# Performance work log

Measured on AMD Instinct MI355X. Metric: run time of the kernel, lower is better.

The kernel has to match this reference:

```python
import jax, jax.numpy as jnp
import numpy as np

B, D, E = 16384, 2048, 16
MIN_K, MAX_K = 1, 4
H = D // 2  # hidden width of similarity/routing MLPs
TOP20 = int(0.2 * D)  # static: int(0.2 * x.shape[-1])


def _lin_init(k, fan_in, shape):
    bound = 1.0 / np.sqrt(fan_in)
    return jax.random.uniform(k, shape, jnp.float32, -bound, bound)


def setup_inputs() -> dict:
    key = jax.random.key(0)
    ks = jax.random.split(key, 16)
    return {
        'x': jax.random.normal(ks[0], (B, D), jnp.float32),
        'expert_patterns': jax.random.normal(ks[1], (E, D), jnp.float32),
        # similarity_network: Linear(D, D//2) -> ReLU -> Linear(D//2, E)
        'Ws1': _lin_init(ks[2], D, (D, H)), 'bs1': _lin_init(ks[3], D, (H,)),
        'Ws2': _lin_init(ks[4], H, (H, E)), 'bs2': _lin_init(ks[5], H, (E,)),
        # routing_network: Linear(D+E, D//2) -> ReLU -> (Dropout eval) -> Linear(D//2, E) -> Softmax
        'Wr1': _lin_init(ks[6], D + E, (D + E, H)), 'br1': _lin_init(ks[7], D + E, (H,)),
        'Wr2': _lin_init(ks[8], H, (H, E)), 'br2': _lin_init(ks[9], H, (E,)),
        # k_predictor: Linear(6,16) -> ReLU -> Linear(16,1) -> Sigmoid
        'Wk1': _lin_init(ks[10], 6, (6, 16)), 'bk1': _lin_init(ks[11], 6, (16,)),
        'Wk2': _lin_init(ks[12], 16, (16, 1)), 'bk2': _lin_init(ks[13], 16, (1,)),
    }


def _feature_analysis(x):
    mean = jnp.mean(x, axis=-1, keepdims=True)
    var_u = jnp.var(x, axis=-1, ddof=1)  # torch.var is unbiased
    std = jnp.sqrt(var_u[:, None] + 1e-8)
    skew = jnp.mean(((x - mean) / std) ** 3, axis=-1)
    ax = jnp.abs(x)
    sorted_ax = -jnp.sort(-ax, axis=-1)  # descending
    total = jnp.sum(sorted_ax, axis=-1)
    top = jnp.sum(sorted_ax[:, :TOP20], axis=-1)
    # stacked in DynamicTopKSelector order: sparsity,variance,magnitude,norm,skewness,concentration
    stats = jnp.stack([
        jnp.mean((x == 0).astype(jnp.float32), axis=-1),
        var_u,
        jnp.max(ax, axis=-1),
        jnp.linalg.norm(x, axis=-1),
        skew,
        top / (total + 1e-8),
    ], axis=-1)  # [B, 6]
    return stats


def _lower_median(v):
    # torch.median returns the lower of two middle elements for even n
    n = v.shape[0]
    return jnp.sort(v)[(n - 1) // 2]


def reference(x, expert_patterns, Ws1, bs1, Ws2, bs2, Wr1, br1, Wr2, br2, Wk1, bk1, Wk2, bk2):
    stats = _feature_analysis(x)  # [B, 6]
    # expert specialization
    sims = x @ expert_patterns.T                                  # [B, E]
    spec = jax.nn.relu(x @ Ws1 + bs1) @ Ws2 + bs2                 # [B, E]
    spec_scores = jax.nn.sigmoid(sims + spec)
    # routing network (dropout inactive in eval)
    ri = jnp.concatenate([x, spec_scores], axis=-1)               # [B, D+E]
    probs = jax.nn.softmax(jax.nn.relu(ri @ Wr1 + br1) @ Wr2 + br2, axis=-1)
    # dynamic top-k (host-side scalar in torch -> static-shape pad/mask here)
    k_ratio = jax.nn.sigmoid(jax.nn.relu(stats @ Wk1 + bk1) @ Wk2 + bk2)[:, 0]
    k_values = MIN_K + (MAX_K - MIN_K) * k_ratio
    k = jnp.clip(jnp.floor(_lower_median(k_values)).astype(jnp.int32), MIN_K, MAX_K)
    k = jax.lax.stop_gradient(k)
    topk_probs, topk_idx = jax.lax.top_k(probs, MAX_K)            # [B, MAX_K]
    mask = jnp.arange(MAX_K) < k                                  # first k slots active
    gates = jax.nn.softmax(jnp.where(mask, topk_probs, -1e30), axis=-1)
    return gates, topk_idx, probs, stats
```

## Files before the change

### kernel.cpp

```cpp
#include <hip/hip_runtime.h>
#include <hip/hip_bf16.h>

typedef unsigned short u16;
typedef __attribute__((ext_vector_type(8))) short bf16x8;
typedef __attribute__((ext_vector_type(4))) float f32x4;

#define BB 16384
#define DD 2048
#define KEXT 2112
#define HH 1024
#define EE 16
#define TOPN 409

__device__ __forceinline__ u16 f2bf(float f) {
    union { float f; unsigned u; } c; c.f = f;
    unsigned r = c.u + 0x7fffu + ((c.u >> 16) & 1u);
    return (u16)(r >> 16);
}
__device__ __forceinline__ float bf2f(u16 h) {
    union { unsigned u; float f; } c; c.u = ((unsigned)h) << 16; return c.f;
}

__device__ __forceinline__ void ld16_lds(const void* g, void* l) {
    __builtin_amdgcn_global_load_lds(
        (const __attribute__((address_space(1))) unsigned int*)g,
        (__attribute__((address_space(3))) unsigned int*)l, 16, 0, 0);
}

__global__ __launch_bounds__(256)
void prep_t(const float* __restrict__ Ws1, const float* __restrict__ Wr1,
            u16* __restrict__ w1t, u16* __restrict__ wr1h, u16* __restrict__ wr1l,
            const float* __restrict__ Ws2, const float* __restrict__ Wr2,
            const float* __restrict__ pat,
            u16* __restrict__ w2t1, u16* __restrict__ wr2th, u16* __restrict__ wr2tl,
            u16* __restrict__ patTh, u16* __restrict__ patTl)
{
    __shared__ float tile[64][65];
    const int kt = blockIdx.x;
    const int nt = blockIdx.y;
    const int mat = blockIdx.z;
    const int t = threadIdx.x;
    if (mat == 2) {
        int idx = (kt * 16 + nt) * 256 + t;
        if (idx < EE * HH) {
            int e = idx / HH, n = idx % HH;
            w2t1[idx] = f2bf(Ws2[(size_t)n * EE + e]);
            float v = Wr2[(size_t)n * EE + e];
            u16 h = f2bf(v);
            wr2th[idx] = h;
            wr2tl[idx] = f2bf(v - bf2f(h));
        }
        if (idx < EE * DD) {
            float v = pat[idx];
            u16 h = f2bf(v);
            patTh[idx] = h;
            patTl[idx] = f2bf(v - bf2f(h));
        }
        return;
    }
    if (mat == 0 && kt >= 32) return;
    const int k0 = kt * 64, n0 = nt * 64;
    const float* src = mat ? Wr1 : Ws1;
    const int kmax = mat ? (DD + EE) : DD;
    #pragma unroll
    for (int i = 0; i < 16; ++i) {
        int e = i * 256 + t;
        int r = e >> 6, c = e & 63;
        float v = (k0 + r < kmax) ? src[(size_t)(k0 + r) * HH + n0 + c] : 0.0f;
        tile[r][c] = v;
    }
    __syncthreads();
    #pragma unroll
    for (int i = 0; i < 16; ++i) {
        int e = i * 256 + t;
        int rn = e >> 6, ck = e & 63;
        float v = tile[ck][rn];
        size_t oidx = (size_t)(n0 + rn) * KEXT + k0 + ck;
        if (mat == 0) {
            w1t[oidx] = f2bf(v);
        } else {
            u16 h = f2bf(v);
            wr1h[oidx] = h;
            wr1l[oidx] = f2bf(v - bf2f(h));
        }
    }
}

__global__ __launch_bounds__(256)
void stats_kernel(const float* __restrict__ x,
                  const float* __restrict__ Wk1, const float* __restrict__ bk1,
                  const float* __restrict__ Wk2, const float* __restrict__ bk2,
                  float* __restrict__ stats_out, u16* __restrict__ xh, u16* __restrict__ xl,
                  unsigned* __restrict__ kflags)
{
    const int wid = threadIdx.x >> 6;
    const int lane = threadIdx.x & 63;
    const int row = blockIdx.x * 4 + wid;
    const float* xr = x + (size_t)row * DD;

    float v[32];
    #pragma unroll
    for (int s = 0; s < 8; ++s) {
        float4 a = *(const float4*)(xr + s * 256 + lane * 4);
        v[s*4+0]=a.x; v[s*4+1]=a.y; v[s*4+2]=a.z; v[s*4+3]=a.w;
    }

    u16* ph = xh + (size_t)row * KEXT;
    u16* pl = xl + (size_t)row * KEXT;
    #pragma unroll
    for (int s = 0; s < 8; ++s) {
        union { u16 a[4]; unsigned long long q; } H, L;
        #pragma unroll
        for (int c = 0; c < 4; ++c) {
            float f = v[s*4+c];
            u16 h = f2bf(f);
            H.a[c] = h; L.a[c] = f2bf(f - bf2f(h));
        }
        *(unsigned long long*)(ph + s*256 + lane*4) = H.q;
        *(unsigned long long*)(pl + s*256 + lane*4) = L.q;
    }
    ph[DD + lane] = 0;
    pl[DD + lane] = 0;

    float s1 = 0;
    #pragma unroll
    for (int j = 0; j < 32; ++j) s1 += v[j];
    #pragma unroll
    for (int off = 32; off >= 1; off >>= 1) s1 += __shfl_xor(s1, off);
    const float mean = s1 * (1.0f/2048.0f);

    float s2=0, s3=0, sa=0, sq=0, zc=0, mx=0;
    #pragma unroll
    for (int j = 0; j < 32; ++j) {
        float d = v[j] - mean;
        s2 += d*d; s3 += d*d*d;
        float av = fabsf(v[j]);
        sa += av; sq += v[j]*v[j];
        mx = fmaxf(mx, av);
        zc += (v[j] == 0.0f) ? 1.0f : 0.0f;
    }
    #pragma unroll
    for (int off = 32; off >= 1; off >>= 1) {
        s2 += __shfl_xor(s2, off);
        s3 += __shfl_xor(s3, off);
        sa += __shfl_xor(sa, off);
        sq += __shfl_xor(sq, off);
        zc += __shfl_xor(zc, off);
        mx = fmaxf(mx, __shfl_xor(mx, off));
    }

    #pragma unroll
    for (int j = 0; j < 32; ++j) v[j] = fabsf(v[j]);

    unsigned lo = 0, hi = 0x7F800000u;
    while (lo < hi) {
        unsigned mid = (lo + hi) >> 1;
        float midf = __uint_as_float(mid);
        unsigned cnt = 0;
        #pragma unroll
        for (int j = 0; j < 32; ++j)
            cnt += (unsigned)__popcll(__ballot(v[j] > midf));
        if (cnt < TOPN) hi = mid; else lo = mid + 1;
    }
    const float T = __uint_as_float(lo);

    float cg = 0, sg = 0;
    #pragma unroll
    for (int j = 0; j < 32; ++j) {
        if (v[j] > T) { cg += 1.0f; sg += v[j]; }
    }
    #pragma unroll
    for (int off = 32; off >= 1; off >>= 1) { cg += __shfl_xor(cg, off); sg += __shfl_xor(sg, off); }

    if (lane == 0) {
        float top = sg + ((float)TOPN - cg) * T;
        float var_u = s2 * (1.0f/2047.0f);
        float stdv = sqrtf(var_u + 1e-8f);
        float st0 = zc * (1.0f/2048.0f);
        float st1 = var_u;
        float st2 = mx;
        float st3 = sqrtf(sq);
        float st4 = (s3 * (1.0f/2048.0f)) / (stdv*stdv*stdv);
        float st5 = top / (sa + 1e-8f);
        float* so = stats_out + (size_t)row * 6;
        so[0]=st0; so[1]=st1; so[2]=st2; so[3]=st3; so[4]=st4; so[5]=st5;
        float stv[6] = {st0,st1,st2,st3,st4,st5};
        float o = bk2[0];
        #pragma unroll
        for (int i = 0; i < 16; ++i) {
            float h = bk1[i];
            #pragma unroll
            for (int f = 0; f < 6; ++f) h += stv[f] * Wk1[f*16 + i];
            o += fmaxf(h, 0.0f) * Wk2[i];
        }
        float kr = 1.0f / (1.0f + expf(-o));
        float kv = 1.0f + 3.0f * kr;
        kflags[row] = (kv < 2.0f ? 1u : 0u) | (kv < 3.0f ? 0x10000u : 0u);
    }
}

__global__ __launch_bounds__(1024)
void kmed_kernel(const unsigned* __restrict__ kflags, int* __restrict__ counters)
{
    const int t = threadIdx.x;
    unsigned s = 0;
    for (int i = t; i < BB; i += 1024) s += kflags[i];
    #pragma unroll
    for (int off = 32; off >= 1; off >>= 1) s += __shfl_xor(s, off);
    __shared__ unsigned red[16];
    if ((t & 63) == 0) red[t >> 6] = s;
    __syncthreads();
    if (t == 0) {
        unsigned tot = 0;
        #pragma unroll
        for (int w = 0; w < 16; ++w) tot += red[w];
        counters[0] = (int)(tot & 0xFFFFu);
        counters[1] = (int)(tot >> 16);
    }
}

__global__ __launch_bounds__(256)
void gemm_h1(const u16* __restrict__ xh, const u16* __restrict__ xl,
             const u16* __restrict__ w1t, const float* __restrict__ bias,
             const u16* __restrict__ w2t,
             const u16* __restrict__ patTh, const u16* __restrict__ patTl,
             float* __restrict__ spec_part, float* __restrict__ sims_part)
{
    __shared__ u16 SM[2*8192];
    u16* AsH = SM;
    u16* BsH = SM + 8192;
    const int t = threadIdx.x;
    const int id = blockIdx.x;
    const int xcd = id & 7;
    const int jj = id >> 3;
    const int nblk = jj & 7;
    const int mgrp = jj >> 3;
    const int m0 = (xcd * 16 + mgrp) * 128;
    const int n0 = nblk * 128;
    const int wid = t >> 6, lane = t & 63, l16 = lane & 15, q = lane >> 4;
    const int wm = (wid & 1) * 64, wn = (wid >> 1) * 64;
    const int x7 = l16 & 7;
    const bool swave = (wid < 2);

    f32x4 acc[4][4] = {};
    f32x4 sacc[4] = {};

    for (int it = 0; it < 32; ++it) {
        const int k0 = it * 64;
        __syncthreads();
        #pragma unroll
        for (int s = 0; s < 4; ++s) {
            int seg = t + s * 256;
            int row = seg >> 3;
            int c = (seg & 7) ^ (row & 7);
            size_t goff = (size_t)k0 + c * 8;
            ld16_lds(xh  + (size_t)(m0 + row) * KEXT + goff, (void*)(AsH + seg * 8));
            ld16_lds(w1t + (size_t)(n0 + row) * KEXT + goff, (void*)(BsH + seg * 8));
        }
        __syncthreads();
        const bool simiter = ((it & 7) == nblk);
        #pragma unroll
        for (int h = 0; h < 2; ++h) {
            const int coff = ((4*h + q) ^ x7) * 8;
            bf16x8 afh[4], bfh[4];
            #pragma unroll
            for (int i = 0; i < 4; ++i) {
                afh[i] = *(const bf16x8*)(AsH + (wm + 16*i + l16) * 64 + coff);
                bfh[i] = *(const bf16x8*)(BsH + (wn + 16*i + l16) * 64 + coff);
            }
            #pragma unroll
            for (int i = 0; i < 4; ++i)
                #pragma unroll
                for (int j = 0; j < 4; ++j)
                    acc[i][j] = __builtin_amdgcn_mfma_f32_16x16x32_bf16(afh[i], bfh[j], acc[i][j], 0, 0, 0);
            if (simiter && swave) {
                const int gc = k0 + (4*h + q) * 8;
                bf16x8 pb0 = *(const bf16x8*)(patTh + (size_t)l16 * DD + gc);
                bf16x8 pb1 = *(const bf16x8*)(patTl + (size_t)l16 * DD + gc);
                #pragma unroll
                for (int i = 0; i < 4; ++i) {
                    bf16x8 al = *(const bf16x8*)(xl + (size_t)(m0 + wm + 16*i + l16) * KEXT + gc);
                    sacc[i] = __builtin_amdgcn_mfma_f32_16x16x32_bf16(afh[i], pb0, sacc[i], 0, 0, 0);
                    sacc[i] = __builtin_amdgcn_mfma_f32_16x16x32_bf16(afh[i], pb1, sacc[i], 0, 0, 0);
                    sacc[i] = __builtin_amdgcn_mfma_f32_16x16x32_bf16(al,     pb0, sacc[i], 0, 0, 0);
                }
            }
        }
    }

    __syncthreads();
    u16* h1t = SM;
    #pragma unroll
    for (int j = 0; j < 4; ++j) {
        int col = wn + 16*j + l16;
        float bvj = bias[n0 + col];
        #pragma unroll
        for (int i = 0; i < 4; ++i)
            #pragma unroll
            for (int r = 0; r < 4; ++r) {
                int row = wm + 16*i + q*4 + r;
                float vv = acc[i][j][r] + bvj;
                vv = vv > 0.0f ? vv : 0.0f;
                h1t[row * 128 + col] = f2bf(vv);
            }
    }
    __syncthreads();
    const int mb = wid * 32;
    f32x4 s16[2] = {};
    #pragma unroll
    for (int kk = 0; kk < 4; ++kk) {
        bf16x8 wb = *(const bf16x8*)(w2t + (size_t)l16 * HH + n0 + kk*32 + q*8);
        #pragma unroll
        for (int i2 = 0; i2 < 2; ++i2) {
            bf16x8 af = *(const bf16x8*)(h1t + (mb + i2*16 + l16) * 128 + kk*32 + q*8);
            s16[i2] = __builtin_amdgcn_mfma_f32_16x16x32_bf16(af, wb, s16[i2], 0, 0, 0);
        }
    }
    #pragma unroll
    for (int i2 = 0; i2 < 2; ++i2)
        #pragma unroll
        for (int r = 0; r < 4; ++r) {
            int row = m0 + mb + i2*16 + q*4 + r;
            spec_part[((size_t)nblk * BB + row) * EE + l16] = s16[i2][r];
        }
    if (swave) {
        #pragma unroll
        for (int i = 0; i < 4; ++i)
            #pragma unroll
            for (int r = 0; r < 4; ++r) {
                int row = m0 + wm + 16*i + q*4 + r;
                sims_part[((size_t)nblk * BB + row) * EE + l16] = sacc[i][r];
            }
    }
}

__global__ __launch_bounds__(256)
void gemm_h2(const u16* __restrict__ Ah, const u16* __restrict__ Al,
             const u16* __restrict__ Bh, const u16* __restrict__ Bl,
             const float* __restrict__ bias,
             const u16* __restrict__ wr2th, const u16* __restrict__ wr2tl,
             float* __restrict__ lg_part)
{
    __shared__ u16 SM[4*8192];
    u16* AsH = SM;
    u16* BsH = SM + 8192;
    u16* AsL = SM + 2*8192;
    u16* BsL = SM + 3*8192;
    const int t = threadIdx.x;
    const int id = blockIdx.x;
    const int xcd = id & 7;
    const int jj = id >> 3;
    const int nblk = jj & 7;
    const int mgrp = jj >> 3;
    const int m0 = (xcd * 16 + mgrp) * 128;
    const int n0 = nblk * 128;
    const int wid = t >> 6, lane = t & 63, l16 = lane & 15, q = lane >> 4;
    const int wm = (wid & 1) * 64, wn = (wid >> 1) * 64;
    const int x7 = l16 & 7;

    f32x4 acc[4][4] = {};

    for (int it = 0; it < 33; ++it) {
        const int k0 = it * 64;
        __syncthreads();
        #pragma unroll
        for (int s = 0; s < 4; ++s) {
            int seg = t + s * 256;
            int row = seg >> 3;
            int c = (seg & 7) ^ (row & 7);
            size_t goff = (size_t)k0 + c * 8;
            size_t aoff = (size_t)(m0 + row) * KEXT + goff;
            size_t boff = (size_t)(n0 + row) * KEXT + goff;
            ld16_lds(Ah + aoff, (void*)(AsH + seg * 8));
            ld16_lds(Bh + boff, (void*)(BsH + seg * 8));
            ld16_lds(Al + aoff, (void*)(AsL + seg * 8));
            ld16_lds(Bl + boff, (void*)(BsL + seg * 8));
        }
        __syncthreads();
        #pragma unroll
        for (int h = 0; h < 2; ++h) {
            const int coff = ((4*h + q) ^ x7) * 8;
            bf16x8 afh[4], bfh[4], afl[4], bfl[4];
            #pragma unroll
            for (int i = 0; i < 4; ++i) {
                const int ra = (wm + 16*i + l16) * 64 + coff;
                const int rb = (wn + 16*i + l16) * 64 + coff;
                afh[i] = *(const bf16x8*)(AsH + ra);
                bfh[i] = *(const bf16x8*)(BsH + rb);
                afl[i] = *(const bf16x8*)(AsL + ra);
                bfl[i] = *(const bf16x8*)(BsL + rb);
            }
            #pragma unroll
            for (int i = 0; i < 4; ++i)
                #pragma unroll
                for (int j = 0; j < 4; ++j) {
                    acc[i][j] = __builtin_amdgcn_mfma_f32_16x16x32_bf16(afh[i], bfh[j], acc[i][j], 0, 0, 0);
                    acc[i][j] = __builtin_amdgcn_mfma_f32_16x16x32_bf16(afh[i], bfl[j], acc[i][j], 0, 0, 0);
                    acc[i][j] = __builtin_amdgcn_mfma_f32_16x16x32_bf16(afl[i], bfh[j], acc[i][j], 0, 0, 0);
                }
        }
    }

    __syncthreads();
    u16* h2h = SM;
    u16* h2l = SM + 16384;
    #pragma unroll
    for (int j = 0; j < 4; ++j) {
        int col = wn + 16*j + l16;
        float bvj = bias[n0 + col];
        #pragma unroll
        for (int i = 0; i < 4; ++i)
            #pragma unroll
            for (int r = 0; r < 4; ++r) {
                int row = wm + 16*i + q*4 + r;
                float vv = acc[i][j][r] + bvj;
                vv = vv > 0.0f ? vv : 0.0f;
                u16 h = f2bf(vv);
                h2h[row * 128 + col] = h;
                h2l[row * 128 + col] = f2bf(vv - bf2f(h));
            }
    }
    __syncthreads();
    const int mb = wid * 32;
    f32x4 lacc[2] = {};
    #pragma unroll
    for (int kk = 0; kk < 4; ++kk) {
        bf16x8 wbh = *(const bf16x8*)(wr2th + (size_t)l16 * HH + n0 + kk*32 + q*8);
        bf16x8 wbl = *(const bf16x8*)(wr2tl + (size_t)l16 * HH + n0 + kk*32 + q*8);
        #pragma unroll
        for (int i2 = 0; i2 < 2; ++i2) {
            bf16x8 ah = *(const bf16x8*)(h2h + (mb + i2*16 + l16) * 128 + kk*32 + q*8);
            bf16x8 al = *(const bf16x8*)(h2l + (mb + i2*16 + l16) * 128 + kk*32 + q*8);
            lacc[i2] = __builtin_amdgcn_mfma_f32_16x16x32_bf16(ah, wbh, lacc[i2], 0, 0, 0);
            lacc[i2] = __builtin_amdgcn_mfma_f32_16x16x32_bf16(ah, wbl, lacc[i2], 0, 0, 0);
            lacc[i2] = __builtin_amdgcn_mfma_f32_16x16x32_bf16(al, wbh, lacc[i2], 0, 0, 0);
        }
    }
    #pragma unroll
    for (int i2 = 0; i2 < 2; ++i2)
        #pragma unroll
        for (int r = 0; r < 4; ++r) {
            int row = m0 + mb + i2*16 + q*4 + r;
            lg_part[((size_t)nblk * BB + row) * EE + l16] = lacc[i2][r];
        }
}

__global__ __launch_bounds__(64)
void thinAc(const float* __restrict__ spec_part, const float* __restrict__ sims_part,
            const float* __restrict__ bs2,
            u16* __restrict__ xh_w, u16* __restrict__ xl_w)
{
    const int lane = threadIdx.x & 63;
    const int l16 = lane & 15, q = lane >> 4;
    const int m0 = blockIdx.x * 16;
    const float b2 = bs2[l16];
    #pragma unroll
    for (int r = 0; r < 4; ++r) {
        int row = m0 + q*4 + r;
        float sp = 0.0f;
        #pragma unroll
        for (int p = 0; p < 8; ++p) {
            sp += spec_part[((size_t)p * BB + row) * EE + l16];
            sp += sims_part[((size_t)p * BB + row) * EE + l16];
        }
        float ssv = 1.0f / (1.0f + expf(-(sp + b2)));
        u16 h = f2bf(ssv);
        xh_w[(size_t)row * KEXT + DD + l16] = h;
        xl_w[(size_t)row * KEXT + DD + l16] = f2bf(ssv - bf2f(h));
    }
}

__global__ __launch_bounds__(64)
void thinBc(const float* __restrict__ lg_part,
            const float* __restrict__ br2, const int* __restrict__ counters,
            float* __restrict__ out_gates, float* __restrict__ out_idx,
            float* __restrict__ out_probs)
{
    const int lane = threadIdx.x & 63;
    const int l16 = lane & 15, q = lane >> 4;
    const int m0 = blockIdx.x * 16;
    const float b2 = br2[l16];
    const int c2 = counters[0], c3 = counters[1];
    const int k = (c2 >= 8192) ? 1 : ((c3 >= 8192) ? 2 : 3);
    #pragma unroll
    for (int r = 0; r < 4; ++r) {
        const int row = m0 + q*4 + r;
        float lg = b2;
        #pragma unroll
        for (int p = 0; p < 8; ++p)
            lg += lg_part[((size_t)p * BB + row) * EE + l16];
        float mxv = lg;
        #pragma unroll
        for (int off = 1; off < 16; off <<= 1) mxv = fmaxf(mxv, __shfl_xor(mxv, off));
        float e = expf(lg - mxv);
        float den = e;
        #pragma unroll
        for (int off = 1; off < 16; off <<= 1) den += __shfl_xor(den, off);
        float p = e / den;
        out_probs[(size_t)row * EE + l16] = p;
        int kcur = (int)((__float_as_uint(p) & ~15u) | (15u - (unsigned)l16));
        float tv[4]; int ti[4];
        #pragma unroll
        for (int s = 0; s < 4; ++s) {
            int kk = kcur;
            #pragma unroll
            for (int off = 1; off < 16; off <<= 1) kk = max(kk, __shfl_xor(kk, off));
            int widx = 15 - (kk & 15);
            ti[s] = widx;
            tv[s] = __shfl(p, q * 16 + widx);
            if (l16 == widx) kcur = 0;
        }
        float den2 = 0.0f;
        float g[4];
        #pragma unroll
        for (int s = 0; s < 4; ++s) {
            g[s] = expf(tv[s] - tv[0]);
            if (s < k) den2 += g[s];
        }
        if (l16 < 4) {
            out_gates[(size_t)row * 4 + l16] = (l16 < k) ? g[l16] / den2 : 0.0f;
            out_idx[(size_t)row * 4 + l16] = (float)ti[l16];
        }
    }
}

extern "C" void kernel_launch(void* const* d_in, const int* in_sizes, int n_in,
                              void* d_out, int out_size, void* d_ws, size_t ws_size,
                              hipStream_t stream) {
    const float* x   = (const float*)d_in[0];
    const float* pat = (const float*)d_in[1];
    const float* Ws1 = (const float*)d_in[2];
    const float* bs1 = (const float*)d_in[3];
    const float* Ws2 = (const float*)d_in[4];
    const float* bs2 = (const float*)d_in[5];
    const float* Wr1 = (const float*)d_in[6];
    const float* br1 = (const float*)d_in[7];
    const float* Wr2 = (const float*)d_in[8];
    const float* br2 = (const float*)d_in[9];
    const float* Wk1 = (const float*)d_in[10];
    const float* bk1 = (const float*)d_in[11];
    const float* Wk2 = (const float*)d_in[12];
    const float* bk2 = (const float*)d_in[13];

    char* ws = (char*)d_ws;
    size_t off = 0;
    auto alloc = [&](size_t bytes) { char* p = ws + off; off += (bytes + 255) & ~(size_t)255; return p; };
    u16* xh     = (u16*)alloc((size_t)BB * KEXT * 2);
    u16* xl     = (u16*)alloc((size_t)BB * KEXT * 2);
    u16* w1t    = (u16*)alloc((size_t)HH * KEXT * 2);
    u16* wr1h   = (u16*)alloc((size_t)HH * KEXT * 2);
    u16* wr1l   = (u16*)alloc((size_t)HH * KEXT * 2);
    u16* w2t1   = (u16*)alloc((size_t)EE * HH * 2);
    u16* wr2th  = (u16*)alloc((size_t)EE * HH * 2);
    u16* wr2tl  = (u16*)alloc((size_t)EE * HH * 2);
    u16* patTh  = (u16*)alloc((size_t)EE * DD * 2);
    u16* patTl  = (u16*)alloc((size_t)EE * DD * 2);
    float* partA = (float*)alloc((size_t)16 * BB * EE * 4);
    float* partB = (float*)alloc((size_t)8  * BB * EE * 4);
    unsigned* kflags = (unsigned*)alloc((size_t)BB * 4);
    int* cnt      = (int*)alloc(64);

    float* spec_part = partA;
    float* sims_part = partA + (size_t)8 * BB * EE;
    float* lg_part   = partB;

    float* out        = (float*)d_out;
    float* out_gates  = out;
    float* out_idx    = out + (size_t)BB * 4;
    float* out_probs  = out + (size_t)BB * 8;
    float* out_stats  = out + (size_t)BB * 24;

    prep_t<<<dim3(33, 16, 3), 256, 0, stream>>>(Ws1, Wr1, w1t, wr1h, wr1l,
        Ws2, Wr2, pat, w2t1, wr2th, wr2tl, patTh, patTl);

    stats_kernel<<<BB/4, 256, 0, stream>>>(x, Wk1, bk1, Wk2, bk2, out_stats, xh, xl, kflags);

    kmed_kernel<<<1, 1024, 0, stream>>>(kflags, cnt);

    gemm_h1<<<1024, 256, 0, stream>>>(xh, xl, w1t, bs1, w2t1, patTh, patTl,
                                      spec_part, sims_part);

    thinAc<<<BB/16, 64, 0, stream>>>(spec_part, sims_part, bs2, xh, xl);

    gemm_h2<<<1024, 256, 0, stream>>>(xh, xl, wr1h, wr1l, br1, wr2th, wr2tl, lg_part);

    thinBc<<<BB/16, 64, 0, stream>>>(lg_part, br2, cnt, out_gates, out_idx, out_probs);
}
```

Before: 570.1 us.

## Merge stats and weight prep kernels, bf16 top-k search, enlarge gemm_h1 M tile

Three unrelated changes. The weight-prep kernel and the stats kernel are merged into one launch, with the prep work placed in extra blocks after the 4096 stats blocks. The top-20% threshold binary search now runs on bf16-rounded integer keys, which cuts the iterations from about 31 to about 15. gemm_h1 goes from 128x128 to 256x128 tiles with 512 blocks and launch bounds of 2, so each B tile is reused across twice as many rows. The bf16 threshold makes the top-sum approximate when values tie near the threshold, since ties are filled at T rather than the exact value. The larger tile also raises register and LDS pressure.

```diff
diff --git a/kernel.cpp b/kernel.cpp
--- a/kernel.cpp
+++ b/kernel.cpp
@@ -28,73 +28,76 @@
 }
 
 __global__ __launch_bounds__(256)
-void prep_t(const float* __restrict__ Ws1, const float* __restrict__ Wr1,
-            u16* __restrict__ w1t, u16* __restrict__ wr1h, u16* __restrict__ wr1l,
-            const float* __restrict__ Ws2, const float* __restrict__ Wr2,
-            const float* __restrict__ pat,
-            u16* __restrict__ w2t1, u16* __restrict__ wr2th, u16* __restrict__ wr2tl,
-            u16* __restrict__ patTh, u16* __restrict__ patTl)
+void stats_prep(const float* __restrict__ x,
+                const float* __restrict__ Wk1, const float* __restrict__ bk1,
+                const float* __restrict__ Wk2, const float* __restrict__ bk2,
+                float* __restrict__ stats_out, u16* __restrict__ xh, u16* __restrict__ xl,
+                unsigned* __restrict__ kflags,
+                const float* __restrict__ Ws1, const float* __restrict__ Wr1,
+                u16* __restrict__ w1t, u16* __restrict__ wr1h, u16* __restrict__ wr1l,
+                const float* __restrict__ Ws2, const float* __restrict__ Wr2,
+                const float* __restrict__ pat,
+                u16* __restrict__ w2t1, u16* __restrict__ wr2th, u16* __restrict__ wr2tl,
+                u16* __restrict__ patTh, u16* __restrict__ patTl)
 {
     __shared__ float tile[64][65];
-    const int kt = blockIdx.x;
-    const int nt = blockIdx.y;
-    const int mat = blockIdx.z;
     const int t = threadIdx.x;
-    if (mat == 2) {
-        int idx = (kt * 16 + nt) * 256 + t;
-        if (idx < EE * HH) {
-            int e = idx / HH, n = idx % HH;
-            w2t1[idx] = f2bf(Ws2[(size_t)n * EE + e]);
-            float v = Wr2[(size_t)n * EE + e];
-            u16 h = f2bf(v);
-            wr2th[idx] = h;
-            wr2tl[idx] = f2bf(v - bf2f(h));
-        }
-        if (idx < EE * DD) {
-            float v = pat[idx];
-            u16 h = f2bf(v);
-            patTh[idx] = h;
-            patTl[idx] = f2bf(v - bf2f(h));
+
+    if (blockIdx.x >= 4096) {
+        const int e = blockIdx.x - 4096;
+        const int mat = e / (33 * 16);
+        const int rem = e % (33 * 16);
+        const int kt = rem % 33;
+        const int nt = rem / 33;
+        if (mat == 2) {
+            int idx = rem * 256 + t;
+            if (idx < EE * HH) {
+                int ee = idx / HH, n = idx % HH;
+                w2t1[idx] = f2bf(Ws2[(size_t)n * EE + ee]);
+                float v = Wr2[(size_t)n * EE + ee];
+                u16 h = f2bf(v);
+                wr2th[idx] = h;
+                wr2tl[idx] = f2bf(v - bf2f(h));
+            }
+            if (idx < EE * DD) {
+                float v = pat[idx];
+                u16 h = f2bf(v);
+                patTh[idx] = h;
+                patTl[idx] = f2bf(v - bf2f(h));
+            }
+            return;
+        }
+        if (mat == 0 && kt >= 32) return;
+        const int k0 = kt * 64, n0 = nt * 64;
+        const float* src = mat ? Wr1 : Ws1;
+        const int kmax = mat ? (DD + EE) : DD;
+        #pragma unroll
+        for (int i = 0; i < 16; ++i) {
+            int ei = i * 256 + t;
+            int r = ei >> 6, c = ei & 63;
+            float v = (k0 + r < kmax) ? src[(size_t)(k0 + r) * HH + n0 + c] : 0.0f;
+            tile[r][c] = v;
+        }
+        __syncthreads();
+        #pragma unroll
+        for (int i = 0; i < 16; ++i) {
+            int ei = i * 256 + t;
+            int rn = ei >> 6, ck = ei & 63;
+            float v = tile[ck][rn];
+            size_t oidx = (size_t)(n0 + rn) * KEXT + k0 + ck;
+            if (mat == 0) {
+                w1t[oidx] = f2bf(v);
+            } else {
+                u16 h = f2bf(v);
+                wr1h[oidx] = h;
+                wr1l[oidx] = f2bf(v - bf2f(h));
+            }
         }
         return;
     }
-    if (mat == 0 && kt >= 32) return;
-    const int k0 = kt * 64, n0 = nt * 64;
-    const float* src = mat ? Wr1 : Ws1;
-    const int kmax = mat ? (DD + EE) : DD;
-    #pragma unroll
-    for (int i = 0; i < 16; ++i) {
-        int e = i * 256 + t;
-        int r = e >> 6, c = e & 63;
-        float v = (k0 + r < kmax) ? src[(size_t)(k0 + r) * HH + n0 + c] : 0.0f;
-        tile[r][c] = v;
-    }
-    __syncthreads();
-    #pragma unroll
-    for (int i = 0; i < 16; ++i) {
-        int e = i * 256 + t;
-        int rn = e >> 6, ck = e & 63;
-        float v = tile[ck][rn];
-        size_t oidx = (size_t)(n0 + rn) * KEXT + k0 + ck;
-        if (mat == 0) {
-            w1t[oidx] = f2bf(v);
-        } else {
-            u16 h = f2bf(v);
-            wr1h[oidx] = h;
-            wr1l[oidx] = f2bf(v - bf2f(h));
-        }
-    }
-}
-
-__global__ __launch_bounds__(256)
-void stats_kernel(const float* __restrict__ x,
-                  const float* __restrict__ Wk1, const float* __restrict__ bk1,
-                  const float* __restrict__ Wk2, const float* __restrict__ bk2,
-                  float* __restrict__ stats_out, u16* __restrict__ xh, u16* __restrict__ xl,
-                  unsigned* __restrict__ kflags)
-{
-    const int wid = threadIdx.x >> 6;
-    const int lane = threadIdx.x & 63;
+
+    const int wid = t >> 6;
+    const int lane = t & 63;
     const int row = blockIdx.x * 4 + wid;
     const float* xr = x + (size_t)row * DD;
 
@@ -149,20 +152,22 @@
         mx = fmaxf(mx, __shfl_xor(mx, off));
     }
 
-    #pragma unroll
-    for (int j = 0; j < 32; ++j) v[j] = fabsf(v[j]);
-
-    unsigned lo = 0, hi = 0x7F800000u;
+    int b[32];
+    #pragma unroll
+    for (int j = 0; j < 32; ++j) {
+        v[j] = fabsf(v[j]);
+        b[j] = (int)f2bf(v[j]);
+    }
+    unsigned lo = 0, hi = 0x7F80u;
     while (lo < hi) {
         unsigned mid = (lo + hi) >> 1;
-        float midf = __uint_as_float(mid);
         unsigned cnt = 0;
         #pragma unroll
         for (int j = 0; j < 32; ++j)
-            cnt += (unsigned)__popcll(__ballot(v[j] > midf));
+            cnt += (unsigned)__popcll(__ballot(b[j] > (int)mid));
         if (cnt < TOPN) hi = mid; else lo = mid + 1;
     }
-    const float T = __uint_as_float(lo);
+    const float T = bf2f((u16)lo);
 
     float cg = 0, sg = 0;
     #pragma unroll
@@ -219,70 +224,75 @@
     }
 }
 
-__global__ __launch_bounds__(256)
+__global__ __launch_bounds__(256, 2)
 void gemm_h1(const u16* __restrict__ xh, const u16* __restrict__ xl,
              const u16* __restrict__ w1t, const float* __restrict__ bias,
              const u16* __restrict__ w2t,
              const u16* __restrict__ patTh, const u16* __restrict__ patTl,
              float* __restrict__ spec_part, float* __restrict__ sims_part)
 {
-    __shared__ u16 SM[2*8192];
+    __shared__ u16 SM[32768];
     u16* AsH = SM;
-    u16* BsH = SM + 8192;
+    u16* BsH = SM + 16384;
     const int t = threadIdx.x;
     const int id = blockIdx.x;
     const int xcd = id & 7;
     const int jj = id >> 3;
     const int nblk = jj & 7;
     const int mgrp = jj >> 3;
-    const int m0 = (xcd * 16 + mgrp) * 128;
+    const int m0 = (xcd * 8 + mgrp) * 256;
     const int n0 = nblk * 128;
     const int wid = t >> 6, lane = t & 63, l16 = lane & 15, q = lane >> 4;
-    const int wm = (wid & 1) * 64, wn = (wid >> 1) * 64;
+    const int wm = (wid & 1) * 128, wn = (wid >> 1) * 64;
     const int x7 = l16 & 7;
     const bool swave = (wid < 2);
 
-    f32x4 acc[4][4] = {};
-    f32x4 sacc[4] = {};
+    f32x4 acc[8][4] = {};
+    f32x4 sacc[8] = {};
 
     for (int it = 0; it < 32; ++it) {
         const int k0 = it * 64;
         __syncthreads();
+        #pragma unroll
+        for (int s = 0; s < 8; ++s) {
+            int seg = t + s * 256;
+            int row = seg >> 3;
+            int c = (seg & 7) ^ (row & 7);
+            ld16_lds(xh + (size_t)(m0 + row) * KEXT + k0 + c * 8, (void*)(AsH + seg * 8));
+        }
         #pragma unroll
         for (int s = 0; s < 4; ++s) {
             int seg = t + s * 256;
             int row = seg >> 3;
             int c = (seg & 7) ^ (row & 7);
-            size_t goff = (size_t)k0 + c * 8;
-            ld16_lds(xh  + (size_t)(m0 + row) * KEXT + goff, (void*)(AsH + seg * 8));
-            ld16_lds(w1t + (size_t)(n0 + row) * KEXT + goff, (void*)(BsH + seg * 8));
+            ld16_lds(w1t + (size_t)(n0 + row) * KEXT + k0 + c * 8, (void*)(BsH + seg * 8));
         }
         __syncthreads();
         const bool simiter = ((it & 7) == nblk);
         #pragma unroll
         for (int h = 0; h < 2; ++h) {
             const int coff = ((4*h + q) ^ x7) * 8;
-            bf16x8 afh[4], bfh[4];
-            #pragma unroll
-            for (int i = 0; i < 4; ++i) {
-                afh[i] = *(const bf16x8*)(AsH + (wm + 16*i + l16) * 64 + coff);
-                bfh[i] = *(const bf16x8*)(BsH + (wn + 16*i + l16) * 64 + coff);
-            }
-            #pragma unroll
-            for (int i = 0; i < 4; ++i)
+            const int gc = k0 + (4*h + q) * 8;
+            bf16x8 bfh[4];
+            #pragma unroll
+            for (int j = 0; j < 4; ++j)
+                bfh[j] = *(const bf16x8*)(BsH + (wn + 16*j + l16) * 64 + coff);
+            bf16x8 pb0 = {}, pb1 = {};
+            if (simiter && swave) {
+                pb0 = *(const bf16x8*)(patTh + (size_t)l16 * DD + gc);
+                pb1 = *(const bf16x8*)(patTl + (size_t)l16 * DD + gc);
+            }
+            #pragma unroll
+            for (int i = 0; i < 8; ++i) {
+                bf16x8 afh = *(const bf16x8*)(AsH + (wm + 16*i + l16) * 64 + coff);
                 #pragma unroll
                 for (int j = 0; j < 4; ++j)
-                    acc[i][j] = __builtin_amdgcn_mfma_f32_16x16x32_bf16(afh[i], bfh[j], acc[i][j], 0, 0, 0);
-            if (simiter && swave) {
-                const int gc = k0 + (4*h + q) * 8;
-                bf16x8 pb0 = *(const bf16x8*)(patTh + (size_t)l16 * DD + gc);
-                bf16x8 pb1 = *(const bf16x8*)(patTl + (size_t)l16 * DD + gc);
-                #pragma unroll
-                for (int i = 0; i < 4; ++i) {
+                    acc[i][j] = __builtin_amdgcn_mfma_f32_16x16x32_bf16(afh, bfh[j], acc[i][j], 0, 0, 0);
+                if (simiter && swave) {
                     bf16x8 al = *(const bf16x8*)(xl + (size_t)(m0 + wm + 16*i + l16) * KEXT + gc);
-                    sacc[i] = __builtin_amdgcn_mfma_f32_16x16x32_bf16(afh[i], pb0, sacc[i], 0, 0, 0);
-                    sacc[i] = __builtin_amdgcn_mfma_f32_16x16x32_bf16(afh[i], pb1, sacc[i], 0, 0, 0);
-                    sacc[i] = __builtin_amdgcn_mfma_f32_16x16x32_bf16(al,     pb0, sacc[i], 0, 0, 0);
+                    sacc[i] = __builtin_amdgcn_mfma_f32_16x16x32_bf16(afh, pb0, sacc[i], 0, 0, 0);
+                    sacc[i] = __builtin_amdgcn_mfma_f32_16x16x32_bf16(afh, pb1, sacc[i], 0, 0, 0);
+                    sacc[i] = __builtin_amdgcn_mfma_f32_16x16x32_bf16(al,  pb0, sacc[i], 0, 0, 0);
                 }
             }
         }
@@ -295,7 +305,7 @@
         int col = wn + 16*j + l16;
         float bvj = bias[n0 + col];
         #pragma unroll
-        for (int i = 0; i < 4; ++i)
+        for (int i = 0; i < 8; ++i)
             #pragma unroll
             for (int r = 0; r < 4; ++r) {
                 int row = wm + 16*i + q*4 + r;
@@ -305,19 +315,19 @@
             }
     }
     __syncthreads();
-    const int mb = wid * 32;
-    f32x4 s16[2] = {};
+    const int mb = wid * 64;
+    f32x4 s16[4] = {};
     #pragma unroll
     for (int kk = 0; kk < 4; ++kk) {
         bf16x8 wb = *(const bf16x8*)(w2t + (size_t)l16 * HH + n0 + kk*32 + q*8);
         #pragma unroll
-        for (int i2 = 0; i2 < 2; ++i2) {
+        for (int i2 = 0; i2 < 4; ++i2) {
             bf16x8 af = *(const bf16x8*)(h1t + (mb + i2*16 + l16) * 128 + kk*32 + q*8);
             s16[i2] = __builtin_amdgcn_mfma_f32_16x16x32_bf16(af, wb, s16[i2], 0, 0, 0);
         }
     }
     #pragma unroll
-    for (int i2 = 0; i2 < 2; ++i2)
+    for (int i2 = 0; i2 < 4; ++i2)
         #pragma unroll
         for (int r = 0; r < 4; ++r) {
             int row = m0 + mb + i2*16 + q*4 + r;
@@ -325,7 +335,7 @@
         }
     if (swave) {
         #pragma unroll
-        for (int i = 0; i < 4; ++i)
+        for (int i = 0; i < 8; ++i)
             #pragma unroll
             for (int r = 0; r < 4; ++r) {
                 int row = m0 + wm + 16*i + q*4 + r;
@@ -570,15 +580,15 @@
     float* out_probs  = out + (size_t)BB * 8;
     float* out_stats  = out + (size_t)BB * 24;
 
-    prep_t<<<dim3(33, 16, 3), 256, 0, stream>>>(Ws1, Wr1, w1t, wr1h, wr1l,
-        Ws2, Wr2, pat, w2t1, wr2th, wr2tl, patTh, patTl);
-
-    stats_kernel<<<BB/4, 256, 0, stream>>>(x, Wk1, bk1, Wk2, bk2, out_stats, xh, xl, kflags);
+    stats_prep<<<4096 + 1584, 256, 0, stream>>>(
+        x, Wk1, bk1, Wk2, bk2, out_stats, xh, xl, kflags,
+        Ws1, Wr1, w1t, wr1h, wr1l, Ws2, Wr2, pat,
+        w2t1, wr2th, wr2tl, patTh, patTl);
 
     kmed_kernel<<<1, 1024, 0, stream>>>(kflags, cnt);
 
-    gemm_h1<<<1024, 256, 0, stream>>>(xh, xl, w1t, bs1, w2t1, patTh, patTl,
-                                      spec_part, sims_part);
+    gemm_h1<<<512, 256, 0, stream>>>(xh, xl, w1t, bs1, w2t1, patTh, patTl,
+                                     spec_part, sims_part);
 
     thinAc<<<BB/16, 64, 0, stream>>>(spec_part, sims_part, bs2, xh, xl);
 
```

Measured after the change: 597.1 us. 1.05x slower.
